# Kernel optimization log

Hardware: AMD Instinct MI355X
Metric: run time of the kernel (lower is better)

The kernel has to match this reference:

```python
import jax, jax.numpy as jnp
import numpy as np

# Quantization constants from the original module
X_ZP = -66   # int8 zero point
Y_ZP = 160   # uint8 zero point


def setup_inputs() -> dict:
    key = jax.random.key(0)
    k1, k2 = jax.random.split(key)
    # x: [7, B, M, K] int8 in [-128, 127]
    x = jax.random.randint(k1, (7, 8, 512, 1024), -128, 128, dtype=jnp.int32).astype(jnp.int8)
    # y: [B, K, N] uint8 in [0, 255]
    y = jax.random.randint(k2, (8, 1024, 512), 0, 256, dtype=jnp.int32).astype(jnp.uint8)
    return {
        "x": x,
        "y": y,
        "x_scale": jnp.float32(0.03),
        "y_scale": jnp.float32(0.025),
    }


def reference(x, y, x_scale, y_scale):
    # dequantize_per_tensor: (q - zero_point) * scale
    xf = (x.astype(jnp.float32) - jnp.float32(X_ZP)) * x_scale   # [7, B, M, K]
    yf = (y.astype(jnp.float32) - jnp.float32(Y_ZP)) * y_scale   # [B, K, N]
    # torch.matmul broadcast: [7,B,M,K] @ [B,K,N] -> [7,B,M,N]
    return jnp.einsum('gbmk,bkn->gbmn', xf, yf)
```

## Files before the change

kernel.cpp:

```cpp
#include <hip/hip_runtime.h>
#include <stdint.h>

#define AS1 __attribute__((address_space(1)))
#define AS3 __attribute__((address_space(3)))

typedef int v4i __attribute__((ext_vector_type(4)));

constexpr int G = 7, B = 8, M = 512, N = 512, K = 1024;
constexpr int GBn = G * B;

constexpr size_t X8_BYTES = (size_t)GBn * M * K;
constexpr size_t YT_BYTES = (size_t)B * N * K;
constexpr size_t RS_CNT   = (size_t)GBn * M;
constexpr size_t CS_CNT   = (size_t)B * N;
constexpr size_t WS_NEEDED = X8_BYTES + YT_BYTES + RS_CNT * 4 + CS_CNT * 4;

__global__ __launch_bounds__(256) void transpose_pack_y(const int* __restrict__ y,
                                                        signed char* __restrict__ yt) {
    __shared__ unsigned char tile[64][80];
    int n0 = blockIdx.x * 64;
    int k0 = blockIdx.y * 64;
    int b  = blockIdx.z;
    int t  = threadIdx.x;

    int r  = t >> 2;
    int c0 = (t & 3) * 16;
    const int* src = y + ((size_t)b * K + k0 + r) * N + n0 + c0;
    uint32_t p[4];
#pragma unroll
    for (int q = 0; q < 4; ++q) {
        int4 v = ((const int4*)src)[q];
        p[q] =  (uint32_t)((v.x & 255) ^ 128)
             | ((uint32_t)((v.y & 255) ^ 128) << 8)
             | ((uint32_t)((v.z & 255) ^ 128) << 16)
             | ((uint32_t)((v.w & 255) ^ 128) << 24);
    }
    *(uint4*)&tile[r][c0] = make_uint4(p[0], p[1], p[2], p[3]);
    __syncthreads();

    int nl = t >> 2;
    int kc = (t & 3) * 16;
    uint32_t q[4];
#pragma unroll
    for (int w = 0; w < 4; ++w) {
        uint32_t b0 = tile[kc + w * 4 + 0][nl];
        uint32_t b1 = tile[kc + w * 4 + 1][nl];
        uint32_t b2 = tile[kc + w * 4 + 2][nl];
        uint32_t b3 = tile[kc + w * 4 + 3][nl];
        q[w] = b0 | (b1 << 8) | (b2 << 16) | (b3 << 24);
    }
    *(uint4*)(yt + ((size_t)b * N + n0 + nl) * K + k0 + kc) = make_uint4(q[0], q[1], q[2], q[3]);
}

__device__ __forceinline__ int wave_reduce_sum(int v) {
#pragma unroll
    for (int off = 32; off > 0; off >>= 1) v += __shfl_down(v, off, 64);
    return v;
}

__global__ __launch_bounds__(256) void pack_x_sums(const int* __restrict__ x,
                                                   signed char* __restrict__ x8,
                                                   const signed char* __restrict__ yt,
                                                   int* __restrict__ rowsum,
                                                   int* __restrict__ colsum) {
    int wave = threadIdx.x >> 6, lane = threadIdx.x & 63;
    int row = blockIdx.x * 4 + wave;
    if (row < (int)(GBn * M)) {
        const int* src = x + (size_t)row * K + lane * 16;
        int s = 0;
        uint32_t p[4];
#pragma unroll
        for (int q = 0; q < 4; ++q) {
            int4 v = ((const int4*)src)[q];
            s += v.x + v.y + v.z + v.w;
            p[q] =  (uint32_t)(v.x & 255)
                 | ((uint32_t)(v.y & 255) << 8)
                 | ((uint32_t)(v.z & 255) << 16)
                 | ((uint32_t)(v.w & 255) << 24);
        }
        *(uint4*)(x8 + (size_t)row * K + lane * 16) = make_uint4(p[0], p[1], p[2], p[3]);
        s = wave_reduce_sum(s);
        if (lane == 0) rowsum[row] = s;
    } else {
        int rr = row - (int)(GBn * M);
        uint4 u = *(const uint4*)(yt + (size_t)rr * K + lane * 16);
        uint32_t wds[4] = {u.x, u.y, u.z, u.w};
        int s = 0;
#pragma unroll
        for (int q = 0; q < 4; ++q) {
            uint32_t w = wds[q];
            s += (int)(signed char)(w) + (int)(signed char)(w >> 8)
               + (int)(signed char)(w >> 16) + (int)(signed char)(w >> 24);
        }
        s = wave_reduce_sum(s);
        if (lane == 0) colsum[rr] = s;
    }
}

__global__ __launch_bounds__(256, 2) void gemm_i8(const signed char* __restrict__ x8,
                                                  const signed char* __restrict__ yt,
                                                  const int* __restrict__ rowsum,
                                                  const int* __restrict__ colsum,
                                                  const float* __restrict__ xsp,
                                                  const float* __restrict__ ysp,
                                                  float* __restrict__ out) {
    __shared__ signed char As[128 * 64];
    __shared__ signed char Bs[128 * 64];

    int tile = blockIdx.x;
    int gb   = blockIdx.y;
    int mt = tile >> 2, nt = tile & 3;
    int b  = gb & 7;
    int tid = threadIdx.x, wave = tid >> 6, lane = tid & 63;
    int wm = (wave >> 1) * 64, wn = (wave & 1) * 64;

    int srow  = lane >> 2;
    int sslot = (lane & 3) ^ ((lane >> 3) & 3);
    const signed char* Ab = x8 + ((size_t)(gb * M + mt * 128 + wave * 32 + srow)) * K + sslot * 16;
    const signed char* Bb = yt + ((size_t)(b  * N + nt * 128 + wave * 32 + srow)) * K + sslot * 16;
    signed char* AsW = As + wave * 2048;
    signed char* BsW = Bs + wave * 2048;

    v4i zero = {0, 0, 0, 0};
    v4i acc[4][4];
#pragma unroll
    for (int i = 0; i < 4; ++i)
#pragma unroll
        for (int j = 0; j < 4; ++j) acc[i][j] = zero;

    int fr = lane & 15;
    int fk = ((lane >> 4) ^ ((fr >> 1) & 3)) * 16;

    for (int k0 = 0; k0 < K; k0 += 64) {
#pragma unroll
        for (int c = 0; c < 2; ++c) {
            __builtin_amdgcn_global_load_lds((const AS1 uint32_t*)(Ab + (size_t)c * 16 * K + k0),
                                             (AS3 uint32_t*)(AsW + c * 1024), 16, 0, 0);
            __builtin_amdgcn_global_load_lds((const AS1 uint32_t*)(Bb + (size_t)c * 16 * K + k0),
                                             (AS3 uint32_t*)(BsW + c * 1024), 16, 0, 0);
        }
        __syncthreads();

        v4i af[4], bf[4];
#pragma unroll
        for (int i = 0; i < 4; ++i)
            af[i] = *(const v4i*)(As + (wm + i * 16 + fr) * 64 + fk);
#pragma unroll
        for (int j = 0; j < 4; ++j)
            bf[j] = *(const v4i*)(Bs + (wn + j * 16 + fr) * 64 + fk);

#pragma unroll
        for (int i = 0; i < 4; ++i)
#pragma unroll
            for (int j = 0; j < 4; ++j)
                acc[i][j] = __builtin_amdgcn_mfma_i32_16x16x64_i8(af[i], bf[j], acc[i][j], 0, 0, 0);
        __syncthreads();
    }

    float s = xsp[0] * ysp[0];
    int colL = lane & 15;
    int rowQ = (lane >> 4) * 4;
    float* outg = out + (size_t)gb * M * N;
    const int* rs = rowsum + gb * M;
    const int* cs = colsum + b * N;
#pragma unroll
    for (int i = 0; i < 4; ++i) {
#pragma unroll
        for (int r = 0; r < 4; ++r) {
            int row_g = mt * 128 + wm + i * 16 + rowQ + r;
            int rsv = rs[row_g];
#pragma unroll
            for (int j = 0; j < 4; ++j) {
                int col_g = nt * 128 + wn + j * 16 + colL;
                int t = acc[i][j][r] - 32 * rsv + 66 * cs[col_g] - 2162688;
                outg[(size_t)row_g * N + col_g] = s * (float)t;
            }
        }
    }
}

__global__ __launch_bounds__(256) void naive_kernel(const int* __restrict__ x,
                                                    const int* __restrict__ y,
                                                    const float* __restrict__ xsp,
                                                    const float* __restrict__ ysp,
                                                    float* __restrict__ out) {
    size_t idx = (size_t)blockIdx.x * 256 + threadIdx.x;
    int n  = (int)(idx & 511);
    int m  = (int)((idx >> 9) & 511);
    int gb = (int)(idx >> 18);
    int b  = gb & 7;
    const int* xr = x + ((size_t)gb * M + m) * K;
    const int* yc = y + (size_t)b * K * N + n;
    int dot = 0, sx = 0, sy = 0;
    for (int k = 0; k < K; ++k) {
        int a = xr[k];
        int c = yc[(size_t)k * N];
        dot += a * c; sx += a; sy += c;
    }
    float s = xsp[0] * ysp[0];
    out[idx] = s * (float)(dot - 160 * sx + 66 * sy - 10813440);
}

extern "C" void kernel_launch(void* const* d_in, const int* in_sizes, int n_in,
                              void* d_out, int out_size, void* d_ws, size_t ws_size,
                              hipStream_t stream) {
    const int*   x  = (const int*)d_in[0];
    const int*   y  = (const int*)d_in[1];
    const float* xs = (const float*)d_in[2];
    const float* ys = (const float*)d_in[3];
    float* out = (float*)d_out;

    if (ws_size < WS_NEEDED) {
        naive_kernel<<<(14680064 + 255) / 256, 256, 0, stream>>>(x, y, xs, ys, out);
        return;
    }

    char* ws = (char*)d_ws;
    signed char* x8 = (signed char*)ws;
    signed char* yt = (signed char*)(ws + X8_BYTES);
    int* rowsum = (int*)(ws + X8_BYTES + YT_BYTES);
    int* colsum = rowsum + RS_CNT;

    transpose_pack_y<<<dim3(N / 64, K / 64, B), 256, 0, stream>>>(y, yt);
    pack_x_sums<<<(GBn * M + CS_CNT) / 4, 256, 0, stream>>>(x, x8, yt, rowsum, colsum);
    gemm_i8<<<dim3(16, GBn), 256, 0, stream>>>(x8, yt, rowsum, colsum, xs, ys, out);
}
```

Baseline: 227.3 us.

## Double-buffer B tile in LDS and load A fragments directly from global

The GEMM kernel stops staging A through shared memory and has each lane load its A fragments straight from global memory into registers. Only B is staged in LDS, now double-buffered so the next K-slice is prefetched while MFMAs run on the current one, which removes one barrier per iteration. Launch bounds are raised to allow 4 blocks per SU and the grid is reshaped to 3D so M-tiles sharing a B tile launch adjacently. The risks are uncoalesced, higher-latency direct global loads for A and possible register spilling under the tighter occupancy bound.

```diff
diff --git a/kernel.cpp b/kernel.cpp
--- a/kernel.cpp
+++ b/kernel.cpp
@@ -97,64 +97,65 @@
     }
 }
 
-__global__ __launch_bounds__(256, 2) void gemm_i8(const signed char* __restrict__ x8,
+__global__ __launch_bounds__(256, 4) void gemm_i8(const signed char* __restrict__ x8,
                                                   const signed char* __restrict__ yt,
                                                   const int* __restrict__ rowsum,
                                                   const int* __restrict__ colsum,
                                                   const float* __restrict__ xsp,
                                                   const float* __restrict__ ysp,
                                                   float* __restrict__ out) {
-    __shared__ signed char As[128 * 64];
-    __shared__ signed char Bs[128 * 64];
-
-    int tile = blockIdx.x;
-    int gb   = blockIdx.y;
-    int mt = tile >> 2, nt = tile & 3;
+    __shared__ signed char Bs[2][128 * 64];
+
+    int mt = blockIdx.x;
+    int nt = blockIdx.y;
+    int gb = blockIdx.z;
     int b  = gb & 7;
     int tid = threadIdx.x, wave = tid >> 6, lane = tid & 63;
     int wm = (wave >> 1) * 64, wn = (wave & 1) * 64;
+    int fr = lane & 15;
+    int q  = lane >> 4;
 
     int srow  = lane >> 2;
     int sslot = (lane & 3) ^ ((lane >> 3) & 3);
-    const signed char* Ab = x8 + ((size_t)(gb * M + mt * 128 + wave * 32 + srow)) * K + sslot * 16;
-    const signed char* Bb = yt + ((size_t)(b  * N + nt * 128 + wave * 32 + srow)) * K + sslot * 16;
-    signed char* AsW = As + wave * 2048;
-    signed char* BsW = Bs + wave * 2048;
-
-    v4i zero = {0, 0, 0, 0};
+    const signed char* Bb = yt + ((size_t)(b * N + nt * 128 + wave * 16 + srow)) * K + sslot * 16;
+
+    const signed char* Aq = x8 + ((size_t)(gb * M + mt * 128 + wm + fr)) * K + q * 16;
+
+    int fkB = (q ^ ((fr >> 1) & 3)) * 16;
+
     v4i acc[4][4];
 #pragma unroll
     for (int i = 0; i < 4; ++i)
 #pragma unroll
-        for (int j = 0; j < 4; ++j) acc[i][j] = zero;
-
-    int fr = lane & 15;
-    int fk = ((lane >> 4) ^ ((fr >> 1) & 3)) * 16;
-
-    for (int k0 = 0; k0 < K; k0 += 64) {
-#pragma unroll
-        for (int c = 0; c < 2; ++c) {
-            __builtin_amdgcn_global_load_lds((const AS1 uint32_t*)(Ab + (size_t)c * 16 * K + k0),
-                                             (AS3 uint32_t*)(AsW + c * 1024), 16, 0, 0);
-            __builtin_amdgcn_global_load_lds((const AS1 uint32_t*)(Bb + (size_t)c * 16 * K + k0),
-                                             (AS3 uint32_t*)(BsW + c * 1024), 16, 0, 0);
-        }
+        for (int j = 0; j < 4; ++j) acc[i][j] = (v4i){0, 0, 0, 0};
+
+#pragma unroll
+    for (int c = 0; c < 2; ++c)
+        __builtin_amdgcn_global_load_lds((const AS1 uint32_t*)(Bb + (size_t)c * 64 * K),
+                                         (AS3 uint32_t*)(&Bs[0][0] + c * 4096 + wave * 1024), 16, 0, 0);
+
+    for (int step = 0; step < 16; ++step) {
+        int k0  = step * 64;
+        int cur = step & 1;
         __syncthreads();
-
+        if (step < 15) {
+#pragma unroll
+            for (int c = 0; c < 2; ++c)
+                __builtin_amdgcn_global_load_lds((const AS1 uint32_t*)(Bb + (size_t)c * 64 * K + k0 + 64),
+                                                 (AS3 uint32_t*)(&Bs[cur ^ 1][0] + c * 4096 + wave * 1024), 16, 0, 0);
+        }
         v4i af[4], bf[4];
 #pragma unroll
         for (int i = 0; i < 4; ++i)
-            af[i] = *(const v4i*)(As + (wm + i * 16 + fr) * 64 + fk);
+            af[i] = *(const v4i*)(Aq + (size_t)i * 16 * K + k0);
 #pragma unroll
         for (int j = 0; j < 4; ++j)
-            bf[j] = *(const v4i*)(Bs + (wn + j * 16 + fr) * 64 + fk);
-
+            bf[j] = *(const v4i*)(&Bs[cur][0] + (wn + j * 16 + fr) * 64 + fkB);
 #pragma unroll
         for (int i = 0; i < 4; ++i)
 #pragma unroll
             for (int j = 0; j < 4; ++j)
                 acc[i][j] = __builtin_amdgcn_mfma_i32_16x16x64_i8(af[i], bf[j], acc[i][j], 0, 0, 0);
-        __syncthreads();
     }
 
     float s = xsp[0] * ysp[0];
@@ -223,5 +224,5 @@
 
     transpose_pack_y<<<dim3(N / 64, K / 64, B), 256, 0, stream>>>(y, yt);
     pack_x_sums<<<(GBn * M + CS_CNT) / 4, 256, 0, stream>>>(x, x8, yt, rowsum, colsum);
-    gemm_i8<<<dim3(16, GBn), 256, 0, stream>>>(x8, yt, rowsum, colsum, xs, ys, out);
-}
+    gemm_i8<<<dim3(M / 128, N / 128, GBn), 256, 0, stream>>>(x8, yt, rowsum, colsum, xs, ys, out);
+}
```

Result: slower. 241.4 us (+6.2%).
